# Performance work log

Hardware: AMD Instinct MI355X
Metric: run time of the kernel (lower is better)

Reference implementation:

```python
import jax, jax.numpy as jnp
import numpy as np


def ternarize_weight(w):
    # abs-mean threshold quantization to {-am, 0, +am}
    abs_mean = jnp.maximum(jnp.abs(w).mean(), 1e-5)
    thr = 0.7 * abs_mean
    q = jnp.where(w > thr, 1.0, jnp.where(w < -thr, -1.0, 0.0))
    # STE: forward value is q*abs_mean, grad flows to w as identity
    return w + jax.lax.stop_gradient(q * abs_mean - w)


def rotate_half(x):
    x1, x2 = jnp.split(x, 2, axis=-1)
    return jnp.concatenate([-x2, x1], axis=-1)


def setup_inputs() -> dict:
    key = jax.random.key(0)
    k1, k2, k3, k4, k5 = jax.random.split(key, 5)
    B, T, C, H = 2, 2048, 1024, 16
    D = C // H
    x = jax.random.normal(k1, (B, T, C), dtype=jnp.float32)
    cos = jax.random.uniform(k2, (1, 1, T, D), dtype=jnp.float32)
    sin = jax.random.uniform(k3, (1, 1, T, D), dtype=jnp.float32)
    w_qkv = jax.random.normal(k4, (3 * C, C), dtype=jnp.float32) / np.sqrt(C)
    w_proj = jax.random.normal(k5, (C, C), dtype=jnp.float32) / np.sqrt(C)
    return {"x": x, "cos": cos, "sin": sin, "w_qkv": w_qkv, "w_proj": w_proj}


def reference(x, cos, sin, w_qkv, w_proj):
    B, T, C = x.shape
    H = 16
    D = C // H
    wq = ternarize_weight(w_qkv)
    wp = ternarize_weight(w_proj)
    qkv = x @ wq.T  # [B,T,3C]
    q, k, v = jnp.split(qkv, 3, axis=-1)
    # [B,T,C] -> [B,H,T,D]
    q = q.reshape(B, T, H, D).transpose(0, 2, 1, 3)
    k = k.reshape(B, T, H, D).transpose(0, 2, 1, 3)
    v = v.reshape(B, T, H, D).transpose(0, 2, 1, 3)
    # RoPE
    q = q * cos + rotate_half(q) * sin
    k = k * cos + rotate_half(k) * sin
    # causal SDPA
    scale = 1.0 / np.sqrt(D)
    scores = jnp.einsum("bhqd,bhkd->bhqk", q, k) * scale
    causal = jnp.tril(jnp.ones((T, T), dtype=bool))
    scores = jnp.where(causal, scores, jnp.finfo(scores.dtype).min)
    attn = jax.nn.softmax(scores, axis=-1)
    y = jnp.einsum("bhqk,bhkd->bhqd", attn, v)  # [B,H,T,D]
    y = y.transpose(0, 2, 1, 3).reshape(B, T, C)
    return y @ wp.T
```

## Files before the change

### kernel.cpp

```cpp
#include <hip/hip_runtime.h>
#include <hip/hip_bf16.h>

#define B_ 2
#define T_ 2048
#define C_ 1024
#define H_ 16
#define D_ 64
#define M_ 4096
#define N3C 3072

using short8  = __attribute__((ext_vector_type(8))) short;
using floatx4 = __attribute__((ext_vector_type(4))) float;
typedef unsigned int u32;

__device__ __forceinline__ unsigned short f2b(float f) {
  __hip_bfloat16 h = __float2bfloat16(f);
  return *reinterpret_cast<unsigned short*>(&h);
}
__device__ __forceinline__ float b2f(unsigned short u) {
  union { unsigned int i; float f; } x; x.i = ((unsigned int)u) << 16; return x.f;
}

__device__ __forceinline__ void gll16(const void* g, void* l) {
  __builtin_amdgcn_global_load_lds((const __attribute__((address_space(1))) u32*)g,
                                   (__attribute__((address_space(3))) u32*)l, 16, 0, 0);
}


__global__ void abs_sum2(const float* __restrict__ wq, const float* __restrict__ wp,
                         double* __restrict__ sums) {
  __shared__ double red[4];
  const float* w = blockIdx.y ? wp : wq;
  const int n4 = blockIdx.y ? (C_ * C_ / 4) : (3 * C_ * C_ / 4);
  int stride = gridDim.x * blockDim.x;
  double s = 0.0;
  for (int i = blockIdx.x * blockDim.x + threadIdx.x; i < n4; i += stride) {
    float4 v = ((const float4*)w)[i];
    s += (double)fabsf(v.x) + (double)fabsf(v.y) + (double)fabsf(v.z) + (double)fabsf(v.w);
  }
  #pragma unroll
  for (int off = 32; off > 0; off >>= 1)
    s += __shfl_down(s, off, 64);
  if ((threadIdx.x & 63) == 0) red[threadIdx.x >> 6] = s;
  __syncthreads();
  if (threadIdx.x == 0) atomicAdd(sums + blockIdx.y, (red[0] + red[1]) + (red[2] + red[3]));
}

__global__ void tern_cvt(const float* __restrict__ wq, const float* __restrict__ wp,
                         const float* __restrict__ x,
                         unsigned short* __restrict__ oq, unsigned short* __restrict__ op,
                         unsigned short* __restrict__ xb,
                         const double* __restrict__ sums, float* __restrict__ ams) {
  const int NQ = 3 * C_ * C_;
  const int NP = C_ * C_;
  int i = blockIdx.x * blockDim.x + threadIdx.x;
  float am0 = fmaxf((float)(sums[0] * (1.0 / NQ)), 1e-5f);
  float am1 = fmaxf((float)(sums[1] * (1.0 / NP)), 1e-5f);
  if (i == 0) { ams[0] = am0; ams[1] = am1; }
  if (i < NQ) {
    float thr = 0.7f * am0, v = wq[i];
    oq[i] = (v > thr) ? 0x3F80u : ((v < -thr) ? 0xBF80u : 0u);
  } else if (i < NQ + NP) {
    int j = i - NQ;
    float thr = 0.7f * am1, v = wp[j];
    op[j] = (v > thr) ? 0x3F80u : ((v < -thr) ? 0xBF80u : 0u);
  } else {
    int j = i - NQ - NP;
    float4 v = ((const float4*)x)[j];
    ushort4 o; o.x = f2b(v.x); o.y = f2b(v.y); o.z = f2b(v.z); o.w = f2b(v.w);
    ((ushort4*)xb)[j] = o;
  }
}


__global__ __launch_bounds__(256) void gemm_qkv(const unsigned short* __restrict__ A,
                                                const unsigned short* __restrict__ W,
                                                const float* __restrict__ scale_ptr,
                                                const float* __restrict__ cosp,
                                                const float* __restrict__ sinp,
                                                unsigned short* __restrict__ Qb,
                                                unsigned short* __restrict__ Kb,
                                                unsigned short* __restrict__ Vtb) {
  const int K = C_;
  __shared__ __attribute__((aligned(16))) unsigned short As[128 * 32];
  __shared__ __attribute__((aligned(16))) unsigned short Ws[128 * 32];
  const int tid = threadIdx.x, lane = tid & 63, wv = tid >> 6;
  const int m = lane & 15, g = lane >> 4;
  const int m0 = blockIdx.y * 128, n0 = blockIdx.x * 128;
  const int wm = (wv >> 1) * 64, wn = (wv & 1) * 64;

  const int srow = wv * 16 + (lane >> 2);
  const int skoff = (lane & 3) * 8;
  const unsigned short* ga0 = A + (size_t)(m0 + srow) * K + skoff;
  const unsigned short* ga1 = A + (size_t)(m0 + 64 + srow) * K + skoff;
  const unsigned short* gw0 = W + (size_t)(n0 + srow) * K + skoff;
  const unsigned short* gw1 = W + (size_t)(n0 + 64 + srow) * K + skoff;
  unsigned short* la0 = As + (wv * 16) * 32;
  unsigned short* la1 = As + (64 + wv * 16) * 32;
  unsigned short* lw0 = Ws + (wv * 16) * 32;
  unsigned short* lw1 = Ws + (64 + wv * 16) * 32;

  floatx4 acc[4][4] = {};
  for (int kc = 0; kc < K; kc += 32) {
    __syncthreads();
    gll16(ga0, la0); gll16(ga1, la1); gll16(gw0, lw0); gll16(gw1, lw1);
    ga0 += 32; ga1 += 32; gw0 += 32; gw1 += 32;
    __syncthreads();
    short8 af[4], wf[4];
    #pragma unroll
    for (int r = 0; r < 4; r++)
      af[r] = *(const short8*)&As[(wm + r * 16 + m) * 32 + g * 8];
    #pragma unroll
    for (int c = 0; c < 4; c++)
      wf[c] = *(const short8*)&Ws[(wn + c * 16 + m) * 32 + g * 8];
    #pragma unroll
    for (int r = 0; r < 4; r++)
      #pragma unroll
      for (int c = 0; c < 4; c++)
        acc[r][c] = __builtin_amdgcn_mfma_f32_16x16x32_bf16(af[r], wf[c], acc[r][c], 0, 0, 0);
  }

  const float am = *scale_ptr;
  const int sect = n0 >> 10;
  const int nloc = n0 & 1023;
  const int h = (nloc + wn) >> 6;
  if (sect < 2) {
    unsigned short* dst = sect ? Kb : Qb;
    const float sc = sect ? am : am * 0.18033688011112042f;
    #pragma unroll
    for (int r = 0; r < 4; r++)
      #pragma unroll
      for (int i = 0; i < 4; i++) {
        int row = m0 + wm + r * 16 + g * 4 + i;
        int t = row & (T_ - 1), b = row >> 11;
        size_t obase = ((size_t)(b * H_ + h) * T_ + t) * 64;
        #pragma unroll
        for (int c = 0; c < 4; c++) {
          int p = c * 16 + m;
          float cv = cosp[t * 64 + p], sv = sinp[t * 64 + p];
          float a = acc[r][c][i], pt = acc[r][c ^ 2][i];
          float val = (c < 2) ? (a * cv - pt * sv) : (a * cv + pt * sv);
          dst[obase + p] = f2b(val * sc);
        }
      }
  } else {
    #pragma unroll
    for (int r = 0; r < 4; r++)
      #pragma unroll
      for (int i = 0; i < 4; i++) {
        int row = m0 + wm + r * 16 + g * 4 + i;
        int t = row & (T_ - 1), b = row >> 11;
        size_t hbase = (size_t)(b * H_ + h) * 64 * T_;
        #pragma unroll
        for (int c = 0; c < 4; c++)
          Vtb[hbase + (size_t)(c * 16 + m) * T_ + t] = f2b(acc[r][c][i] * am);
      }
  }
}


__global__ __launch_bounds__(256) void gemm128(const unsigned short* __restrict__ A,
                                               const unsigned short* __restrict__ W,
                                               const float* __restrict__ scale_ptr,
                                               float* __restrict__ Cout,
                                               int N, int K) {
  __shared__ __attribute__((aligned(16))) unsigned short As[128 * 32];
  __shared__ __attribute__((aligned(16))) unsigned short Ws[128 * 32];
  const int tid = threadIdx.x, lane = tid & 63, wv = tid >> 6;
  const int m = lane & 15, g = lane >> 4;
  const int m0 = blockIdx.y * 128, n0 = blockIdx.x * 128;
  const int wm = (wv >> 1) * 64, wn = (wv & 1) * 64;

  const int srow = wv * 16 + (lane >> 2);
  const int skoff = (lane & 3) * 8;
  const unsigned short* ga0 = A + (size_t)(m0 + srow) * K + skoff;
  const unsigned short* ga1 = A + (size_t)(m0 + 64 + srow) * K + skoff;
  const unsigned short* gw0 = W + (size_t)(n0 + srow) * K + skoff;
  const unsigned short* gw1 = W + (size_t)(n0 + 64 + srow) * K + skoff;
  unsigned short* la0 = As + (wv * 16) * 32;
  unsigned short* la1 = As + (64 + wv * 16) * 32;
  unsigned short* lw0 = Ws + (wv * 16) * 32;
  unsigned short* lw1 = Ws + (64 + wv * 16) * 32;

  floatx4 acc[4][4] = {};
  for (int kc = 0; kc < K; kc += 32) {
    __syncthreads();
    gll16(ga0, la0); gll16(ga1, la1); gll16(gw0, lw0); gll16(gw1, lw1);
    ga0 += 32; ga1 += 32; gw0 += 32; gw1 += 32;
    __syncthreads();
    short8 af[4], wf[4];
    #pragma unroll
    for (int r = 0; r < 4; r++)
      af[r] = *(const short8*)&As[(wm + r * 16 + m) * 32 + g * 8];
    #pragma unroll
    for (int c = 0; c < 4; c++)
      wf[c] = *(const short8*)&Ws[(wn + c * 16 + m) * 32 + g * 8];
    #pragma unroll
    for (int r = 0; r < 4; r++)
      #pragma unroll
      for (int c = 0; c < 4; c++)
        acc[r][c] = __builtin_amdgcn_mfma_f32_16x16x32_bf16(af[r], wf[c], acc[r][c], 0, 0, 0);
  }

  const float scale = *scale_ptr;
  #pragma unroll
  for (int r = 0; r < 4; r++)
    #pragma unroll
    for (int c = 0; c < 4; c++)
      #pragma unroll
      for (int i = 0; i < 4; i++) {
        int row = m0 + wm + r * 16 + g * 4 + i;
        int col = n0 + wn + c * 16 + m;
        Cout[(size_t)row * N + col] = acc[r][c][i] * scale;
      }
}


__global__ __launch_bounds__(256) void flash_mfma(const unsigned short* __restrict__ Qb,
                                                  const unsigned short* __restrict__ Kb,
                                                  const unsigned short* __restrict__ Vtb,
                                                  unsigned short* __restrict__ Y) {
  __shared__ __align__(16) unsigned short Ktile[2][64][64];
  __shared__ __align__(16) unsigned short Vtile[2][64][64];
  __shared__ __align__(16) unsigned short Plds[4][16][72];
  const int lane = threadIdx.x & 63;
  const int wv = threadIdx.x >> 6;
  const int m = lane & 15, g = lane >> 4;
  const int gid = blockIdx.x;
  const int xcd = gid & 7, j = gid >> 3;
  const int bh = xcd * 4 + (j & 3);
  const int s = 15 - (j >> 2);
  const int b = bh >> 4, h = bh & 15;
  const size_t hb = (size_t)bh * T_ * 64;
  const unsigned short* Kbh = Kb + hb;
  const unsigned short* Vbh = Vtb + hb;
  const int r8 = lane >> 3, cc8 = lane & 7;
  const int gcol = ((cc8 ^ r8) << 3);

  const int ntiles = 2 * s + 2;
  const int qb0 = s * 128 + wv * 32;
  const int qb1 = qb0 + 16;

  const unsigned short* qp0 = Qb + hb + (size_t)(qb0 + m) * 64 + g * 8;
  short8 qf00 = *(const short8*)qp0;
  short8 qf01 = *(const short8*)(qp0 + 32);
  const unsigned short* qp1 = qp0 + 16 * 64;
  short8 qf10 = *(const short8*)qp1;
  short8 qf11 = *(const short8*)(qp1 + 32);

  floatx4 O0[4] = {}, O1[4] = {};
  float ls0 = 0.f, ls1 = 0.f;

  #pragma unroll
  for (int cc = 0; cc < 2; cc++) {
    int row = wv * 16 + cc * 8;
    gll16(Kbh + (size_t)(row + r8) * 64 + gcol, &Ktile[0][row][0]);
    gll16(Vbh + (size_t)(row + r8) * T_ + gcol, &Vtile[0][row][0]);
  }

  for (int kt = 0; kt < ntiles; kt++) {
    const int buf = kt & 1;
    const int kb = kt * 64;
    __syncthreads();
    if (kt + 1 < ntiles) {
      const int kb2 = kb + 64;
      #pragma unroll
      for (int cc = 0; cc < 2; cc++) {
        int row = wv * 16 + cc * 8;
        gll16(Kbh + (size_t)(kb2 + row + r8) * 64 + gcol, &Ktile[1 - buf][row][0]);
        gll16(Vbh + (size_t)(row + r8) * T_ + kb2 + gcol, &Vtile[1 - buf][row][0]);
      }
    }
    if (kb > qb0 + 31) continue;

    auto do_qset = [&](short8 qa, short8 qb_, int qbase, float& lsum, floatx4* O) {
      floatx4 S[4];
      #pragma unroll
      for (int mt = 0; mt < 4; mt++) {
        int row = mt * 16 + m;
        short8 kf0 = *(const short8*)&Ktile[buf][row][(g ^ (m & 7)) << 3];
        short8 kf1 = *(const short8*)&Ktile[buf][row][((g + 4) ^ (m & 7)) << 3];
        floatx4 sv = {};
        sv = __builtin_amdgcn_mfma_f32_16x16x32_bf16(kf0, qa, sv, 0, 0, 0);
        sv = __builtin_amdgcn_mfma_f32_16x16x32_bf16(kf1, qb_, sv, 0, 0, 0);
        S[mt] = sv;
      }
      if (kb + 64 <= qbase) {
        #pragma unroll
        for (int mt = 0; mt < 4; mt++) {
          float e0 = exp2f(S[mt][0]), e1 = exp2f(S[mt][1]);
          float e2 = exp2f(S[mt][2]), e3 = exp2f(S[mt][3]);
          lsum += (e0 + e1) + (e2 + e3);
          ushort4 o; o.x = f2b(e0); o.y = f2b(e1); o.z = f2b(e2); o.w = f2b(e3);
          *(ushort4*)&Plds[wv][m][mt * 16 + g * 4] = o;
        }
      } else {
        const int q_glob = qbase + m;
        #pragma unroll
        for (int mt = 0; mt < 4; mt++) {
          float e[4];
          #pragma unroll
          for (int r = 0; r < 4; r++) {
            int kg = kb + mt * 16 + g * 4 + r;
            e[r] = (kg <= q_glob) ? exp2f(S[mt][r]) : 0.f;
          }
          lsum += (e[0] + e[1]) + (e[2] + e[3]);
          ushort4 o; o.x = f2b(e[0]); o.y = f2b(e[1]); o.z = f2b(e[2]); o.w = f2b(e[3]);
          *(ushort4*)&Plds[wv][m][mt * 16 + g * 4] = o;
        }
      }
      short8 pa0 = *(const short8*)&Plds[wv][m][g * 8];
      short8 pa1 = *(const short8*)&Plds[wv][m][32 + g * 8];
      #pragma unroll
      for (int nt = 0; nt < 4; nt++) {
        int row = nt * 16 + m;
        short8 v0 = *(const short8*)&Vtile[buf][row][(g ^ (m & 7)) << 3];
        short8 v1 = *(const short8*)&Vtile[buf][row][((g + 4) ^ (m & 7)) << 3];
        O[nt] = __builtin_amdgcn_mfma_f32_16x16x32_bf16(pa0, v0, O[nt], 0, 0, 0);
        O[nt] = __builtin_amdgcn_mfma_f32_16x16x32_bf16(pa1, v1, O[nt], 0, 0, 0);
      }
    };

    do_qset(qf00, qf01, qb0, ls0, O0);
    if (kb <= qb1 + 15) do_qset(qf10, qf11, qb1, ls1, O1);
  }

  #pragma unroll
  for (int jq = 0; jq < 2; jq++) {
    float lsum = jq ? ls1 : ls0;
    floatx4* O = jq ? O1 : O0;
    const int qbase = jq ? qb1 : qb0;
    lsum += __shfl_xor(lsum, 16, 64);
    lsum += __shfl_xor(lsum, 32, 64);
    float li[4];
    #pragma unroll
    for (int r = 0; r < 4; r++) li[r] = 1.0f / __shfl(lsum, g * 4 + r, 64);
    #pragma unroll
    for (int nt = 0; nt < 4; nt++)
      #pragma unroll
      for (int r = 0; r < 4; r++) {
        int trow = qbase + g * 4 + r;
        int col = h * 64 + nt * 16 + m;
        Y[(size_t)(b * T_ + trow) * C_ + col] = f2b(O[nt][r] * li[r]);
      }
  }
}


extern "C" void kernel_launch(void* const* d_in, const int* in_sizes, int n_in,
                              void* d_out, int out_size, void* d_ws, size_t ws_size,
                              hipStream_t stream) {
  (void)in_sizes; (void)n_in; (void)out_size; (void)ws_size;
  const float* x      = (const float*)d_in[0];
  const float* cosp   = (const float*)d_in[1];
  const float* sinp   = (const float*)d_in[2];
  const float* w_qkv  = (const float*)d_in[3];
  const float* w_proj = (const float*)d_in[4];
  float* out = (float*)d_out;

  char* ws = (char*)d_ws;
  double* sums = (double*)ws;
  float*  ams  = (float*)(ws + 16);
  unsigned short* wqkv_b  = (unsigned short*)(ws + 256);
  unsigned short* wproj_b = wqkv_b + (size_t)N3C * C_;
  unsigned short* xb      = wproj_b + (size_t)C_ * C_;
  unsigned short* Qb      = xb + (size_t)M_ * C_;
  unsigned short* Kb      = Qb + (size_t)B_ * H_ * T_ * D_;
  unsigned short* Vtb     = Kb + (size_t)B_ * H_ * T_ * D_;
  unsigned short* yb      = Vtb + (size_t)B_ * H_ * T_ * D_;

  hipMemsetAsync(sums, 0, 16, stream);
  abs_sum2<<<dim3(256, 2), 256, 0, stream>>>(w_qkv, w_proj, sums);
  tern_cvt<<<(4 * C_ * C_ + M_ * C_ / 4) / 256, 256, 0, stream>>>(w_qkv, w_proj, x,
                                                                  wqkv_b, wproj_b, xb,
                                                                  sums, ams);
  gemm_qkv<<<dim3(N3C / 128, M_ / 128), 256, 0, stream>>>(xb, wqkv_b, ams + 0,
                                                          cosp, sinp, Qb, Kb, Vtb);
  flash_mfma<<<512, 256, 0, stream>>>(Qb, Kb, Vtb, yb);
  gemm128<<<dim3(C_ / 128, M_ / 128), 256, 0, stream>>>(yb, wproj_b, ams + 1, out, C_, C_);
}
```

Measured before the change: 227.1 us.

## Halve flash query tile and proj GEMM N-tile to double block counts

Flash attention now gives each wave 16 query rows (64 per block) and launches 1024 blocks instead of 512. The row-sum of P is computed with an MFMA against a vector of ones instead of scalar adds and shuffles, and the bf16 packing of P uses a paired conversion. The output-projection GEMM uses a 128x64 tile, which doubles its grid. The aim is more parallelism and less tail imbalance on the many compute units, at the cost of reloading K/V tiles for twice as many blocks and rounding the row-sum through bf16 P.

```diff
diff --git a/kernel.cpp b/kernel.cpp
--- a/kernel.cpp
+++ b/kernel.cpp
@@ -19,6 +19,11 @@
 }
 __device__ __forceinline__ float b2f(unsigned short u) {
   union { unsigned int i; float f; } x; x.i = ((unsigned int)u) << 16; return x.f;
+}
+__device__ __forceinline__ u32 pk2(float a, float b) {
+  float2 t; t.x = a; t.y = b;
+  __hip_bfloat162 p = __float22bfloat162_rn(t);
+  return *reinterpret_cast<u32*>(&p);
 }
 
 __device__ __forceinline__ void gll16(const void* g, void* l) {
@@ -159,46 +164,44 @@
 }
 
 
-__global__ __launch_bounds__(256) void gemm128(const unsigned short* __restrict__ A,
-                                               const unsigned short* __restrict__ W,
-                                               const float* __restrict__ scale_ptr,
-                                               float* __restrict__ Cout,
-                                               int N, int K) {
+__global__ __launch_bounds__(256) void gemm_proj(const unsigned short* __restrict__ A,
+                                                 const unsigned short* __restrict__ W,
+                                                 const float* __restrict__ scale_ptr,
+                                                 float* __restrict__ Cout) {
+  const int K = C_, N = C_;
   __shared__ __attribute__((aligned(16))) unsigned short As[128 * 32];
-  __shared__ __attribute__((aligned(16))) unsigned short Ws[128 * 32];
+  __shared__ __attribute__((aligned(16))) unsigned short Ws[64 * 32];
   const int tid = threadIdx.x, lane = tid & 63, wv = tid >> 6;
   const int m = lane & 15, g = lane >> 4;
-  const int m0 = blockIdx.y * 128, n0 = blockIdx.x * 128;
-  const int wm = (wv >> 1) * 64, wn = (wv & 1) * 64;
+  const int m0 = blockIdx.y * 128, n0 = blockIdx.x * 64;
+  const int wm = (wv >> 1) * 64, wn = (wv & 1) * 32;
 
   const int srow = wv * 16 + (lane >> 2);
   const int skoff = (lane & 3) * 8;
   const unsigned short* ga0 = A + (size_t)(m0 + srow) * K + skoff;
   const unsigned short* ga1 = A + (size_t)(m0 + 64 + srow) * K + skoff;
   const unsigned short* gw0 = W + (size_t)(n0 + srow) * K + skoff;
-  const unsigned short* gw1 = W + (size_t)(n0 + 64 + srow) * K + skoff;
   unsigned short* la0 = As + (wv * 16) * 32;
   unsigned short* la1 = As + (64 + wv * 16) * 32;
   unsigned short* lw0 = Ws + (wv * 16) * 32;
-  unsigned short* lw1 = Ws + (64 + wv * 16) * 32;
-
-  floatx4 acc[4][4] = {};
+
+  floatx4 acc[4][2] = {};
   for (int kc = 0; kc < K; kc += 32) {
     __syncthreads();
-    gll16(ga0, la0); gll16(ga1, la1); gll16(gw0, lw0); gll16(gw1, lw1);
-    ga0 += 32; ga1 += 32; gw0 += 32; gw1 += 32;
-    __syncthreads();
-    short8 af[4], wf[4];
+    gll16(ga0, la0); gll16(ga1, la1); gll16(gw0, lw0);
+    ga0 += 32; ga1 += 32; gw0 += 32;
+    __syncthreads();
+    short8 af[4], wf[2];
     #pragma unroll
     for (int r = 0; r < 4; r++)
       af[r] = *(const short8*)&As[(wm + r * 16 + m) * 32 + g * 8];
     #pragma unroll
-    for (int c = 0; c < 4; c++)
+    for (int c = 0; c < 2; c++)
       wf[c] = *(const short8*)&Ws[(wn + c * 16 + m) * 32 + g * 8];
     #pragma unroll
     for (int r = 0; r < 4; r++)
       #pragma unroll
-      for (int c = 0; c < 4; c++)
+      for (int c = 0; c < 2; c++)
         acc[r][c] = __builtin_amdgcn_mfma_f32_16x16x32_bf16(af[r], wf[c], acc[r][c], 0, 0, 0);
   }
 
@@ -206,7 +209,7 @@
   #pragma unroll
   for (int r = 0; r < 4; r++)
     #pragma unroll
-    for (int c = 0; c < 4; c++)
+    for (int c = 0; c < 2; c++)
       #pragma unroll
       for (int i = 0; i < 4; i++) {
         int row = m0 + wm + r * 16 + g * 4 + i;
@@ -229,7 +232,7 @@
   const int gid = blockIdx.x;
   const int xcd = gid & 7, j = gid >> 3;
   const int bh = xcd * 4 + (j & 3);
-  const int s = 15 - (j >> 2);
+  const int s = 31 - (j >> 2);
   const int b = bh >> 4, h = bh & 15;
   const size_t hb = (size_t)bh * T_ * 64;
   const unsigned short* Kbh = Kb + hb;
@@ -237,19 +240,20 @@
   const int r8 = lane >> 3, cc8 = lane & 7;
   const int gcol = ((cc8 ^ r8) << 3);
 
-  const int ntiles = 2 * s + 2;
-  const int qb0 = s * 128 + wv * 32;
-  const int qb1 = qb0 + 16;
-
-  const unsigned short* qp0 = Qb + hb + (size_t)(qb0 + m) * 64 + g * 8;
-  short8 qf00 = *(const short8*)qp0;
-  short8 qf01 = *(const short8*)(qp0 + 32);
-  const unsigned short* qp1 = qp0 + 16 * 64;
-  short8 qf10 = *(const short8*)qp1;
-  short8 qf11 = *(const short8*)(qp1 + 32);
-
-  floatx4 O0[4] = {}, O1[4] = {};
-  float ls0 = 0.f, ls1 = 0.f;
+  const int ntiles = s + 1;
+  const int qbase = s * 64 + wv * 16;
+  const int q_glob = qbase + m;
+
+  const unsigned short* qp = Qb + hb + (size_t)(qbase + m) * 64 + g * 8;
+  short8 qf0 = *(const short8*)qp;
+  short8 qf1 = *(const short8*)(qp + 32);
+
+  short8 ones;
+  #pragma unroll
+  for (int i = 0; i < 8; i++) ones[i] = (short)0x3F80;
+
+  floatx4 O[4] = {};
+  floatx4 accl = {};
 
   #pragma unroll
   for (int cc = 0; cc < 2; cc++) {
@@ -271,79 +275,65 @@
         gll16(Vbh + (size_t)(row + r8) * T_ + kb2 + gcol, &Vtile[1 - buf][row][0]);
       }
     }
-    if (kb > qb0 + 31) continue;
-
-    auto do_qset = [&](short8 qa, short8 qb_, int qbase, float& lsum, floatx4* O) {
-      floatx4 S[4];
+    floatx4 S[4];
+    #pragma unroll
+    for (int mt = 0; mt < 4; mt++) {
+      int row = mt * 16 + m;
+      short8 kf0 = *(const short8*)&Ktile[buf][row][(g ^ (m & 7)) << 3];
+      short8 kf1 = *(const short8*)&Ktile[buf][row][((g + 4) ^ (m & 7)) << 3];
+      floatx4 sv = {};
+      sv = __builtin_amdgcn_mfma_f32_16x16x32_bf16(kf0, qf0, sv, 0, 0, 0);
+      sv = __builtin_amdgcn_mfma_f32_16x16x32_bf16(kf1, qf1, sv, 0, 0, 0);
+      S[mt] = sv;
+    }
+    if (kt + 1 < ntiles) {
       #pragma unroll
       for (int mt = 0; mt < 4; mt++) {
-        int row = mt * 16 + m;
-        short8 kf0 = *(const short8*)&Ktile[buf][row][(g ^ (m & 7)) << 3];
-        short8 kf1 = *(const short8*)&Ktile[buf][row][((g + 4) ^ (m & 7)) << 3];
-        floatx4 sv = {};
-        sv = __builtin_amdgcn_mfma_f32_16x16x32_bf16(kf0, qa, sv, 0, 0, 0);
-        sv = __builtin_amdgcn_mfma_f32_16x16x32_bf16(kf1, qb_, sv, 0, 0, 0);
-        S[mt] = sv;
-      }
-      if (kb + 64 <= qbase) {
+        uint2 w;
+        w.x = pk2(exp2f(S[mt][0]), exp2f(S[mt][1]));
+        w.y = pk2(exp2f(S[mt][2]), exp2f(S[mt][3]));
+        *(uint2*)&Plds[wv][m][mt * 16 + g * 4] = w;
+      }
+    } else {
+      #pragma unroll
+      for (int mt = 0; mt < 4; mt++) {
+        float e[4];
         #pragma unroll
-        for (int mt = 0; mt < 4; mt++) {
-          float e0 = exp2f(S[mt][0]), e1 = exp2f(S[mt][1]);
-          float e2 = exp2f(S[mt][2]), e3 = exp2f(S[mt][3]);
-          lsum += (e0 + e1) + (e2 + e3);
-          ushort4 o; o.x = f2b(e0); o.y = f2b(e1); o.z = f2b(e2); o.w = f2b(e3);
-          *(ushort4*)&Plds[wv][m][mt * 16 + g * 4] = o;
+        for (int r = 0; r < 4; r++) {
+          int kg = kb + mt * 16 + g * 4 + r;
+          e[r] = (kg <= q_glob) ? exp2f(S[mt][r]) : 0.f;
         }
-      } else {
-        const int q_glob = qbase + m;
-        #pragma unroll
-        for (int mt = 0; mt < 4; mt++) {
-          float e[4];
-          #pragma unroll
-          for (int r = 0; r < 4; r++) {
-            int kg = kb + mt * 16 + g * 4 + r;
-            e[r] = (kg <= q_glob) ? exp2f(S[mt][r]) : 0.f;
-          }
-          lsum += (e[0] + e[1]) + (e[2] + e[3]);
-          ushort4 o; o.x = f2b(e[0]); o.y = f2b(e[1]); o.z = f2b(e[2]); o.w = f2b(e[3]);
-          *(ushort4*)&Plds[wv][m][mt * 16 + g * 4] = o;
-        }
-      }
-      short8 pa0 = *(const short8*)&Plds[wv][m][g * 8];
-      short8 pa1 = *(const short8*)&Plds[wv][m][32 + g * 8];
-      #pragma unroll
-      for (int nt = 0; nt < 4; nt++) {
-        int row = nt * 16 + m;
-        short8 v0 = *(const short8*)&Vtile[buf][row][(g ^ (m & 7)) << 3];
-        short8 v1 = *(const short8*)&Vtile[buf][row][((g + 4) ^ (m & 7)) << 3];
-        O[nt] = __builtin_amdgcn_mfma_f32_16x16x32_bf16(pa0, v0, O[nt], 0, 0, 0);
-        O[nt] = __builtin_amdgcn_mfma_f32_16x16x32_bf16(pa1, v1, O[nt], 0, 0, 0);
-      }
-    };
-
-    do_qset(qf00, qf01, qb0, ls0, O0);
-    if (kb <= qb1 + 15) do_qset(qf10, qf11, qb1, ls1, O1);
-  }
-
-  #pragma unroll
-  for (int jq = 0; jq < 2; jq++) {
-    float lsum = jq ? ls1 : ls0;
-    floatx4* O = jq ? O1 : O0;
-    const int qbase = jq ? qb1 : qb0;
-    lsum += __shfl_xor(lsum, 16, 64);
-    lsum += __shfl_xor(lsum, 32, 64);
-    float li[4];
-    #pragma unroll
-    for (int r = 0; r < 4; r++) li[r] = 1.0f / __shfl(lsum, g * 4 + r, 64);
-    #pragma unroll
-    for (int nt = 0; nt < 4; nt++)
-      #pragma unroll
-      for (int r = 0; r < 4; r++) {
-        int trow = qbase + g * 4 + r;
-        int col = h * 64 + nt * 16 + m;
-        Y[(size_t)(b * T_ + trow) * C_ + col] = f2b(O[nt][r] * li[r]);
-      }
-  }
+        uint2 w;
+        w.x = pk2(e[0], e[1]);
+        w.y = pk2(e[2], e[3]);
+        *(uint2*)&Plds[wv][m][mt * 16 + g * 4] = w;
+      }
+    }
+    short8 pa0 = *(const short8*)&Plds[wv][m][g * 8];
+    short8 pa1 = *(const short8*)&Plds[wv][m][32 + g * 8];
+    #pragma unroll
+    for (int nt = 0; nt < 4; nt++) {
+      int row = nt * 16 + m;
+      short8 v0 = *(const short8*)&Vtile[buf][row][(g ^ (m & 7)) << 3];
+      short8 v1 = *(const short8*)&Vtile[buf][row][((g + 4) ^ (m & 7)) << 3];
+      O[nt] = __builtin_amdgcn_mfma_f32_16x16x32_bf16(pa0, v0, O[nt], 0, 0, 0);
+      O[nt] = __builtin_amdgcn_mfma_f32_16x16x32_bf16(pa1, v1, O[nt], 0, 0, 0);
+    }
+    accl = __builtin_amdgcn_mfma_f32_16x16x32_bf16(pa0, ones, accl, 0, 0, 0);
+    accl = __builtin_amdgcn_mfma_f32_16x16x32_bf16(pa1, ones, accl, 0, 0, 0);
+  }
+
+  float li[4];
+  #pragma unroll
+  for (int r = 0; r < 4; r++) li[r] = 1.0f / accl[r];
+  #pragma unroll
+  for (int nt = 0; nt < 4; nt++)
+    #pragma unroll
+    for (int r = 0; r < 4; r++) {
+      int trow = qbase + g * 4 + r;
+      int col = h * 64 + nt * 16 + m;
+      Y[(size_t)(b * T_ + trow) * C_ + col] = f2b(O[nt][r] * li[r]);
+    }
 }
 
 
@@ -376,6 +366,6 @@
                                                                   sums, ams);
   gemm_qkv<<<dim3(N3C / 128, M_ / 128), 256, 0, stream>>>(xb, wqkv_b, ams + 0,
                                                           cosp, sinp, Qb, Kb, Vtb);
-  flash_mfma<<<512, 256, 0, stream>>>(Qb, Kb, Vtb, yb);
-  gemm128<<<dim3(C_ / 128, M_ / 128), 256, 0, stream>>>(yb, wproj_b, ams + 1, out, C_, C_);
-}
+  flash_mfma<<<1024, 256, 0, stream>>>(Qb, Kb, Vtb, yb);
+  gemm_proj<<<dim3(C_ / 64, M_ / 128), 256, 0, stream>>>(yb, wproj_b, ams + 1, out);
+}
```

After: 207.2 us. -8.8%, faster.
